# Performance work log

Measured on AMD Instinct MI355X. Metric: run time of the kernel, lower is better.

## Reference

```python
import jax, jax.numpy as jnp
import numpy as np

S, B, D, H, FF = 1024, 8, 512, 8, 2048
HD = D // H
ALPHA, BETA = 0.5, 0.5
EPS = 1e-5


def setup_inputs() -> dict:
    key = jax.random.key(0)
    ks = jax.random.split(key, 12)
    rn = lambda k, sh, sc=0.02: jax.random.normal(k, sh, dtype=jnp.float32) * sc
    ln = jnp.stack([jnp.ones(D), jnp.zeros(D), jnp.ones(D), jnp.zeros(D)]).astype(jnp.float32)
    return {
        "src": rn(ks[0], (S, B, D), 1.0),
        "src_depth": rn(ks[1], (S, B, D), 1.0),
        "pos": rn(ks[2], (S, B, D), 1.0),
        "attn_w_img": rn(ks[3], (4, D, D)),
        "attn_b_img": jnp.zeros((4, D), jnp.float32),
        "attn_w_dpt": rn(ks[4], (4, D, D)),
        "attn_b_dpt": jnp.zeros((4, D), jnp.float32),
        "ffn_w1_img": rn(ks[5], (FF, D)),
        "ffn_b1_img": jnp.zeros((FF,), jnp.float32),
        "ffn_w2_img": rn(ks[6], (D, FF)),
        "ffn_b2_img": jnp.zeros((D,), jnp.float32),
        "ffn_w1_dpt": rn(ks[7], (FF, D)),
        "ffn_b1_dpt": jnp.zeros((FF,), jnp.float32),
        "ffn_w2_dpt": rn(ks[8], (D, FF)),
        "ffn_b2_dpt": jnp.zeros((D,), jnp.float32),
        "ln_img": ln,
        "ln_dpt": ln,
    }


def _layer_norm(x, g, b):
    m = jnp.mean(x, axis=-1, keepdims=True)
    v = jnp.var(x, axis=-1, keepdims=True)  # biased, matches torch LayerNorm
    return (x - m) * jax.lax.rsqrt(v + EPS) * g + b


def _heads(t, W, b):  # [B,S,D] x [D,D] -> [B,H,S,hd]  (torch Linear: y = x W^T + b)
    y = jnp.einsum('bsd,ed->bse', t, W) + b
    return y.reshape(B, S, H, HD).transpose(0, 2, 1, 3)


def _forward(src, src_depth, pos, attn_w_img, attn_b_img, attn_w_dpt, attn_b_dpt,
             ffn_w1_img, ffn_b1_img, ffn_w2_img, ffn_b2_img,
             ffn_w1_dpt, ffn_b1_dpt, ffn_w2_dpt, ffn_b2_dpt, ln_img, ln_dpt):
    # seq-first -> batch-first
    x = src.transpose(1, 0, 2)        # [B,S,D]
    xd = src_depth.transpose(1, 0, 2)
    p = pos.transpose(1, 0, 2)
    qk_in = x + p                     # img stream: q = k = src + pos
    # depth stream: pos_depth is None in layer.forward -> no pos embed
    q = _heads(qk_in, attn_w_img[0], attn_b_img[0])
    k = _heads(qk_in, attn_w_img[1], attn_b_img[1])
    v = _heads(x, attn_w_img[2], attn_b_img[2])
    qd = _heads(xd, attn_w_dpt[0], attn_b_dpt[0])
    kd = _heads(xd, attn_w_dpt[1], attn_b_dpt[1])
    vd = _heads(xd, attn_w_dpt[2], attn_b_dpt[2])
    scale = 1.0 / np.sqrt(HD).astype(np.float32)
    a_img = jax.nn.softmax(jnp.einsum('bhld,bhsd->bhls', q, k) * scale, axis=-1)
    a_dpt = jax.nn.softmax(jnp.einsum('bhld,bhsd->bhls', qd, kd) * scale, axis=-1)
    sh_img = (1.0 - ALPHA) * a_img + ALPHA * a_dpt
    sh_dpt = (1.0 - BETA) * a_dpt + BETA * a_img
    o_img = jnp.einsum('bhls,bhsd->bhld', sh_img, v).transpose(0, 2, 1, 3).reshape(B, S, D)
    o_dpt = jnp.einsum('bhls,bhsd->bhld', sh_dpt, vd).transpose(0, 2, 1, 3).reshape(B, S, D)
    o_img = jnp.einsum('bsd,ed->bse', o_img, attn_w_img[3]) + attn_b_img[3]
    o_dpt = jnp.einsum('bsd,ed->bse', o_dpt, attn_w_dpt[3]) + attn_b_dpt[3]
    # img residual + LN + FFN + LN
    x = _layer_norm(x + o_img, ln_img[0], ln_img[1])
    ff = jnp.einsum('bsf,df->bsd',
                    jax.nn.relu(jnp.einsum('bsd,fd->bsf', x, ffn_w1_img) + ffn_b1_img),
                    ffn_w2_img) + ffn_b2_img
    x = _layer_norm(x + ff, ln_img[2], ln_img[3])
    # depth residual + LN + FFN + LN
    xd = _layer_norm(xd + o_dpt, ln_dpt[0], ln_dpt[1])
    ffd = jnp.einsum('bsf,df->bsd',
                     jax.nn.relu(jnp.einsum('bsd,fd->bsf', xd, ffn_w1_dpt) + ffn_b1_dpt),
                     ffn_w2_dpt) + ffn_b2_dpt
    xd = _layer_norm(xd + ffd, ln_dpt[2], ln_dpt[3])
    return x.transpose(1, 0, 2), xd.transpose(1, 0, 2)  # back to [S,B,D]


def reference(src, src_depth, pos, attn_w_img, attn_b_img, attn_w_dpt, attn_b_dpt,
              ffn_w1_img, ffn_b1_img, ffn_w2_img, ffn_b2_img,
              ffn_w1_dpt, ffn_b1_dpt, ffn_w2_dpt, ffn_b2_dpt, ln_img, ln_dpt):
    return _forward(src, src_depth, pos, attn_w_img, attn_b_img, attn_w_dpt, attn_b_dpt,
                    ffn_w1_img, ffn_b1_img, ffn_w2_img, ffn_b2_img,
                    ffn_w1_dpt, ffn_b1_dpt, ffn_w2_dpt, ffn_b2_dpt, ln_img, ln_dpt)
```

## Files before the change

### kernel.cpp

```cpp
#include <hip/hip_runtime.h>
#include <math.h>

#define S_  1024
#define B_  8
#define D_  512
#define H_  8
#define HD_ 64
#define FF_ 2048
#define M_  8192
#define DD_ (D_ * D_)

typedef __attribute__((ext_vector_type(8))) short short8;
typedef __attribute__((ext_vector_type(4))) float f32x4;

static __device__ __forceinline__ unsigned short f2bf(float x) {
  union { float f; unsigned int u; } v; v.f = x;
  unsigned int r = v.u + 0x7fff + ((v.u >> 16) & 1);
  return (unsigned short)(r >> 16);
}
static __device__ __forceinline__ float bf2f(unsigned short x) {
  union { unsigned int u; float f; } v; v.u = ((unsigned int)x) << 16;
  return v.f;
}
static __device__ __forceinline__ unsigned int pack_bf2(float a, float b) {
  union { float f; unsigned int u; } x, y; x.f = a; y.f = b;
  return ((x.u + 0x8000u) >> 16) | ((y.u + 0x8000u) & 0xffff0000u);
}
static __device__ __forceinline__ void gl_lds16(const unsigned short* g, unsigned short* l) {
  __builtin_amdgcn_global_load_lds((__attribute__((address_space(1))) void*)(g),
                                   (__attribute__((address_space(3))) void*)(l), 16, 0, 0);
}

struct CvtJobs { const float* in[6]; unsigned short* out[6]; };
__global__ __launch_bounds__(256) void wcvt_kernel(CvtJobs j) {
  int job = blockIdx.y;
  int i = (blockIdx.x * 256 + threadIdx.x) * 4;
  float4 v = *(const float4*)(j.in[job] + i);
  unsigned short u[4] = {f2bf(v.x), f2bf(v.y), f2bf(v.z), f2bf(v.w)};
  *(uint2*)(j.out[job] + i) = *(const uint2*)u;
}

__global__ __launch_bounds__(256) void acvt_kernel(const float* __restrict__ src,
    const float* __restrict__ srcd, const float* __restrict__ pos,
    unsigned short* __restrict__ src16, unsigned short* __restrict__ srcd16,
    unsigned short* __restrict__ qkin16) {
  int job = blockIdx.y;
  int i = (blockIdx.x * 256 + threadIdx.x) * 4;
  const float* a = (job == 0) ? src : (job == 1) ? srcd : src;
  float4 v = *(const float4*)(a + i);
  if (job == 2) {
    float4 p = *(const float4*)(pos + i);
    v.x += p.x; v.y += p.y; v.z += p.z; v.w += p.w;
  }
  unsigned short* o = (job == 0) ? src16 : (job == 1) ? srcd16 : qkin16;
  unsigned short u[4] = {f2bf(v.x), f2bf(v.y), f2bf(v.z), f2bf(v.w)};
  *(uint2*)(o + i) = *(const uint2*)u;
}

static __device__ __forceinline__ void mgemm_body(
    const unsigned short* __restrict__ X, const unsigned short* __restrict__ W,
    const float* __restrict__ bias, const float* __restrict__ resf,
    const unsigned short* __restrict__ resb, unsigned short* __restrict__ Yb,
    float* __restrict__ Yf, int N, int K, int relu, int bx, int by,
    unsigned short* As, unsigned short* Bs)
{
  int tid = threadIdx.x;
  int lane = tid & 63, w = tid >> 6;
  int ml = lane & 15, g = lane >> 4;
  int wm = w >> 1, wn = w & 1;
  int m0 = by * 128, n0 = bx * 128;

  int lrow = w * 32 + (lane >> 2);
  int lcol = (lane & 3) * 8;
  const unsigned short* gA = X + (size_t)(m0 + lrow) * K + lcol;
  const unsigned short* gB = W + (size_t)(n0 + lrow) * K + lcol;
  unsigned short* lA = As + w * 1024;
  unsigned short* lB = Bs + w * 1024;

  f32x4 acc[4][4];
  #pragma unroll
  for (int i = 0; i < 4; i++)
    #pragma unroll
    for (int j = 0; j < 4; j++) acc[i][j] = (f32x4){0.f, 0.f, 0.f, 0.f};

  for (int k0 = 0; k0 < K; k0 += 32) {
    __syncthreads();
    gl_lds16(gA + k0, lA);
    gl_lds16(gA + k0 + (size_t)16 * K, lA + 512);
    gl_lds16(gB + k0, lB);
    gl_lds16(gB + k0 + (size_t)16 * K, lB + 512);
    __syncthreads();

    short8 af[4], bfr[4];
    #pragma unroll
    for (int i = 0; i < 4; i++)
      af[i] = *(const short8*)&As[(wm * 64 + i * 16 + ml) * 32 + g * 8];
    #pragma unroll
    for (int j = 0; j < 4; j++)
      bfr[j] = *(const short8*)&Bs[(wn * 64 + j * 16 + ml) * 32 + g * 8];
    #pragma unroll
    for (int i = 0; i < 4; i++)
      #pragma unroll
      for (int j = 0; j < 4; j++)
        acc[i][j] = __builtin_amdgcn_mfma_f32_16x16x32_bf16(af[i], bfr[j], acc[i][j], 0, 0, 0);
  }

  #pragma unroll
  for (int i = 0; i < 4; i++) {
    int grow = m0 + wm * 64 + i * 16 + g * 4;
    #pragma unroll
    for (int j = 0; j < 4; j++) {
      int gcol = n0 + wn * 64 + j * 16 + ml;
      float bv = bias[gcol];
      #pragma unroll
      for (int r = 0; r < 4; r++) {
        size_t idx = (size_t)(grow + r) * N + gcol;
        float v = acc[i][j][r] + bv;
        if (resf) v += resf[idx];
        if (resb) v += bf2f(resb[idx]);
        if (relu) v = fmaxf(v, 0.0f);
        if (Yb) Yb[idx] = f2bf(v);
        if (Yf) Yf[idx] = v;
      }
    }
  }
}

__global__ __launch_bounds__(256) void qkv_kernel(
    const unsigned short* __restrict__ qkin, const unsigned short* __restrict__ src16,
    const unsigned short* __restrict__ srcd16,
    const unsigned short* __restrict__ w_i, const unsigned short* __restrict__ w_d,
    const float* __restrict__ bA_i, const float* __restrict__ bA_d,
    unsigned short* __restrict__ qkimg, unsigned short* __restrict__ vimg,
    unsigned short* __restrict__ dptqkv)
{
  __shared__ unsigned short As[128 * 32];
  __shared__ unsigned short Bs[128 * 32];
  int bx = blockIdx.x, by = blockIdx.y;
  if (bx < 8)
    mgemm_body(qkin, w_i, bA_i, nullptr, nullptr, qkimg, nullptr, 1024, 512, 0, bx, by, As, Bs);
  else if (bx < 12)
    mgemm_body(src16, w_i + 2 * DD_, bA_i + 1024, nullptr, nullptr, vimg, nullptr, 512, 512, 0, bx - 8, by, As, Bs);
  else
    mgemm_body(srcd16, w_d, bA_d, nullptr, nullptr, dptqkv, nullptr, 1536, 512, 0, bx - 12, by, As, Bs);
}

__global__ __launch_bounds__(256) void pgemm_kernel(
    const unsigned short* __restrict__ X0, const unsigned short* __restrict__ X1,
    const unsigned short* __restrict__ W0, const unsigned short* __restrict__ W1,
    const float* __restrict__ b0, const float* __restrict__ b1,
    const float* __restrict__ rf0, const float* __restrict__ rf1,
    const unsigned short* __restrict__ rb0, const unsigned short* __restrict__ rb1,
    unsigned short* __restrict__ Y0, unsigned short* __restrict__ Y1,
    int N, int K, int relu)
{
  __shared__ unsigned short As[128 * 32];
  __shared__ unsigned short Bs[128 * 32];
  int z = blockIdx.z;
  mgemm_body(z ? X1 : X0, z ? W1 : W0, z ? b1 : b0, z ? rf1 : rf0,
             z ? rb1 : rb0, z ? Y1 : Y0, nullptr, N, K, relu,
             blockIdx.x, blockIdx.y, As, Bs);
}

__global__ __launch_bounds__(256) void vtrans_kernel(
    const unsigned short* __restrict__ v0, int ld0, unsigned short* __restrict__ vt0,
    const unsigned short* __restrict__ v1, int ld1, unsigned short* __restrict__ vt1)
{
  __shared__ unsigned short tile[64][72];
  const unsigned short* v = blockIdx.z ? v1 : v0;
  unsigned short* vt = blockIdx.z ? vt1 : vt0;
  int ld = blockIdx.z ? ld1 : ld0;
  int bh = blockIdx.y, b = bh >> 3, h = bh & 7;
  int s0 = blockIdx.x * 64;
  int tid = threadIdx.x;
  #pragma unroll
  for (int t = 0; t < 2; t++) {
    int idx = t * 256 + tid;
    int i = idx >> 3, c8 = (idx & 7) * 8;
    *(uint4*)&tile[i][c8] =
        *(const uint4*)(v + ((size_t)(s0 + i) * B_ + b) * ld + h * HD_ + c8);
  }
  __syncthreads();
  int hd = tid >> 2, j0 = (tid & 3) * 16;
  unsigned short tmp[16];
  #pragma unroll
  for (int j = 0; j < 16; j++) tmp[j] = tile[j0 + j][hd];
  unsigned short* dst = vt + ((size_t)bh * HD_ + hd) * S_ + s0 + j0;
  *(uint4*)(dst) = *(const uint4*)&tmp[0];
  *(uint4*)(dst + 8) = *(const uint4*)&tmp[8];
}

__global__ __launch_bounds__(256) void ln16_kernel(
    const unsigned short* __restrict__ X0, const unsigned short* __restrict__ X1,
    unsigned short* __restrict__ Yb0, unsigned short* __restrict__ Yb1,
    float* __restrict__ Yf0, float* __restrict__ Yf1,
    const float* __restrict__ gb0, const float* __restrict__ gb1)
{
  int row = blockIdx.x, tid = threadIdx.x;
  int strm = row >> 13, r = row & 8191;
  const unsigned short* X = strm ? X1 : X0;
  unsigned short* Yb = strm ? Yb1 : Yb0;
  float* Yf = strm ? Yf1 : Yf0;
  const float* gb = strm ? gb1 : gb0;

  ushort2 xv = *(const ushort2*)(X + (size_t)r * D_ + 2 * tid);
  float v0 = bf2f(xv.x), v1 = bf2f(xv.y);
  float s = v0 + v1, q = v0 * v0 + v1 * v1;
  #pragma unroll
  for (int msk = 1; msk < 64; msk <<= 1) {
    s += __shfl_xor(s, msk);
    q += __shfl_xor(q, msk);
  }
  __shared__ float ss[4], qs[4];
  int wid = tid >> 6;
  if ((tid & 63) == 0) { ss[wid] = s; qs[wid] = q; }
  __syncthreads();
  s = ss[0] + ss[1] + ss[2] + ss[3];
  q = qs[0] + qs[1] + qs[2] + qs[3];
  float mean = s * (1.0f / D_);
  float var  = q * (1.0f / D_) - mean * mean;
  float inv  = rsqrtf(var + 1e-5f);
  float2 gg = *(const float2*)(gb + 2 * tid);
  float2 bb = *(const float2*)(gb + 512 + 2 * tid);
  float o0 = (v0 - mean) * inv * gg.x + bb.x;
  float o1 = (v1 - mean) * inv * gg.y + bb.y;
  if (Yb) {
    unsigned int pk = pack_bf2(o0, o1);
    unsigned short u[2] = {f2bf(o0), f2bf(o1)};
    *(unsigned int*)(Yb + (size_t)r * D_ + 2 * tid) = *(const unsigned int*)u;
    (void)pk;
  }
  if (Yf) {
    float2 o; o.x = o0; o.y = o1;
    *(float2*)(Yf + (size_t)r * D_ + 2 * tid) = o;
  }
}

__global__ __launch_bounds__(256, 2) void attn_kernel(
    const unsigned short* __restrict__ Qi, const unsigned short* __restrict__ Ki, int ldi,
    const unsigned short* __restrict__ Vti,
    const unsigned short* __restrict__ Qd, const unsigned short* __restrict__ Kd, int ldd,
    const unsigned short* __restrict__ Vtd,
    unsigned short* __restrict__ oi, unsigned short* __restrict__ od)
{
  __shared__ __align__(16) unsigned short Kls[2][64 * 64];
  __shared__ __align__(16) unsigned short Vls[2][64 * 64];
  __shared__ __align__(16) unsigned short Pl[4][2][16 * 80];

  int tid = threadIdx.x;
  int bh = blockIdx.y, b = bh >> 3, h = bh & 7;
  int q0 = blockIdx.x * 128;
  int lane = tid & 63, w = tid >> 6;
  int ml = lane & 15, g = lane >> 4;
  int mx = ml & 7;

  short8 qf[2][2][2];
  #pragma unroll
  for (int t = 0; t < 2; t++) {
    size_t tok = (size_t)(q0 + w * 32 + t * 16 + ml) * B_ + b;
    const unsigned short* qa_i = Qi + tok * ldi + h * HD_ + g * 8;
    const unsigned short* qa_d = Qd + tok * ldd + h * HD_ + g * 8;
    qf[t][0][0] = *(const short8*)(qa_i);  qf[t][0][1] = *(const short8*)(qa_i + 32);
    qf[t][1][0] = *(const short8*)(qa_d);  qf[t][1][1] = *(const short8*)(qa_d + 32);
  }

  int srow = lane >> 3;
  int chg = (lane & 7) ^ srow;
  const unsigned short* gbase; size_t s1, s2; unsigned short* lbase;
  if (w == 0)      { gbase = Ki  + ((size_t)srow * B_ + b) * ldi + h * HD_ + chg * 8; s1 = (size_t)B_ * ldi; s2 = s1; lbase = &Kls[0][0]; }
  else if (w == 1) { gbase = Kd  + ((size_t)srow * B_ + b) * ldd + h * HD_ + chg * 8; s1 = (size_t)B_ * ldd; s2 = s1; lbase = &Kls[1][0]; }
  else if (w == 2) { gbase = Vti + (size_t)bh * HD_ * S_ + (size_t)srow * S_ + chg * 8; s1 = S_; s2 = 1; lbase = &Vls[0][0]; }
  else             { gbase = Vtd + (size_t)bh * HD_ * S_ + (size_t)srow * S_ + chg * 8; s1 = S_; s2 = 1; lbase = &Vls[1][0]; }

  f32x4 acc4[2][4][4];
  #pragma unroll
  for (int t = 0; t < 2; t++)
    #pragma unroll
    for (int cb = 0; cb < 4; cb++)
      #pragma unroll
      for (int n = 0; n < 4; n++) acc4[t][cb][n] = (f32x4){0.f, 0.f, 0.f, 0.f};
  float lI[2] = {0.f, 0.f}, lD[2] = {0.f, 0.f};
  const float scale = 0.125f;

  for (int kt = 0; kt < S_ / 64; kt++) {
    int k0 = kt * 64;
    __syncthreads();
    {
      const unsigned short* gp = gbase + (size_t)k0 * s2;
      #pragma unroll
      for (int rr = 0; rr < 8; rr++)
        gl_lds16(gp + (size_t)rr * 8 * s1, lbase + rr * 512);
    }
    __syncthreads();

    #pragma unroll
    for (int t = 0; t < 2; t++) {
      #pragma unroll
      for (int st = 0; st < 2; st++) {
        float* ls = st ? &lD[t] : &lI[t];
        const unsigned short* Kt = &Kls[st][0];
        #pragma unroll
        for (int n = 0; n < 4; n++) {
          int rbase = (n * 16 + ml) * 64;
          short8 kf0 = *(const short8*)&Kt[rbase + ((g ^ mx) * 8)];
          short8 kf1 = *(const short8*)&Kt[rbase + (((g + 4) ^ mx) * 8)];
          f32x4 a = (f32x4){0.f, 0.f, 0.f, 0.f};
          a = __builtin_amdgcn_mfma_f32_16x16x32_bf16(kf0, qf[t][st][0], a, 0, 0, 0);
          a = __builtin_amdgcn_mfma_f32_16x16x32_bf16(kf1, qf[t][st][1], a, 0, 0, 0);
          float p0 = __expf(a[0] * scale), p1 = __expf(a[1] * scale);
          float p2 = __expf(a[2] * scale), p3 = __expf(a[3] * scale);
          *ls += (p0 + p1) + (p2 + p3);
          uint2 pk; pk.x = pack_bf2(p0, p1); pk.y = pack_bf2(p2, p3);
          *(uint2*)&Pl[w][st][ml * 80 + n * 16 + g * 4] = pk;
        }
      }
      #pragma unroll
      for (int c = 0; c < 2; c++) {
        short8 pI = *(const short8*)&Pl[w][0][ml * 80 + g * 8 + c * 32];
        short8 pD = *(const short8*)&Pl[w][1][ml * 80 + g * 8 + c * 32];
        #pragma unroll
        for (int n = 0; n < 4; n++) {
          int rbase = (n * 16 + ml) * 64;
          int sc = (((g + 4 * c) ^ mx)) * 8;
          short8 vI = *(const short8*)&Vls[0][rbase + sc];
          short8 vD = *(const short8*)&Vls[1][rbase + sc];
          acc4[t][0][n] = __builtin_amdgcn_mfma_f32_16x16x32_bf16(pI, vI, acc4[t][0][n], 0, 0, 0);
          acc4[t][1][n] = __builtin_amdgcn_mfma_f32_16x16x32_bf16(pD, vI, acc4[t][1][n], 0, 0, 0);
          acc4[t][2][n] = __builtin_amdgcn_mfma_f32_16x16x32_bf16(pI, vD, acc4[t][2][n], 0, 0, 0);
          acc4[t][3][n] = __builtin_amdgcn_mfma_f32_16x16x32_bf16(pD, vD, acc4[t][3][n], 0, 0, 0);
        }
      }
    }
  }

  #pragma unroll
  for (int t = 0; t < 2; t++) {
    lI[t] += __shfl_xor(lI[t], 16);  lI[t] += __shfl_xor(lI[t], 32);
    lD[t] += __shfl_xor(lD[t], 16);  lD[t] += __shfl_xor(lD[t], 32);
  }
  #pragma unroll
  for (int t = 0; t < 2; t++) {
    float invI = 1.0f / lI[t], invD = 1.0f / lD[t];
    #pragma unroll
    for (int r = 0; r < 4; r++) {
      float iI = __shfl(invI, g * 4 + r, 16);
      float iD = __shfl(invD, g * 4 + r, 16);
      int qrow = q0 + w * 32 + t * 16 + g * 4 + r;
      size_t ob = ((size_t)qrow * B_ + b) * D_ + h * HD_;
      #pragma unroll
      for (int n = 0; n < 4; n++) {
        oi[ob + n * 16 + ml] = f2bf(0.5f * (acc4[t][0][n][r] * iI + acc4[t][1][n][r] * iD));
        od[ob + n * 16 + ml] = f2bf(0.5f * (acc4[t][3][n][r] * iD + acc4[t][2][n][r] * iI));
      }
    }
  }
}

extern "C" void kernel_launch(void* const* d_in, const int* in_sizes, int n_in,
                              void* d_out, int out_size, void* d_ws, size_t ws_size,
                              hipStream_t stream) {
  const float* src  = (const float*)d_in[0];
  const float* srcd = (const float*)d_in[1];
  const float* pos  = (const float*)d_in[2];
  const float* wA_i = (const float*)d_in[3];
  const float* bA_i = (const float*)d_in[4];
  const float* wA_d = (const float*)d_in[5];
  const float* bA_d = (const float*)d_in[6];
  const float* w1_i = (const float*)d_in[7];
  const float* b1_i = (const float*)d_in[8];
  const float* w2_i = (const float*)d_in[9];
  const float* b2_i = (const float*)d_in[10];
  const float* w1_d = (const float*)d_in[11];
  const float* b1_d = (const float*)d_in[12];
  const float* w2_d = (const float*)d_in[13];
  const float* b2_d = (const float*)d_in[14];
  const float* ln_i = (const float*)d_in[15];
  const float* ln_d = (const float*)d_in[16];

  float* out = (float*)d_out;
  unsigned short* u = (unsigned short*)d_ws;
  const size_t T4 = (size_t)M_ * D_;
  const size_t WSZ = (size_t)FF_ * D_;

  unsigned short* src16  = u;
  unsigned short* srcd16 = u + T4;
  unsigned short* qkimg  = u + 2 * T4;
  unsigned short* vimg   = u + 4 * T4;
  unsigned short* dptqkv = u + 5 * T4;
  unsigned short* w_i16  = u + 8 * T4;
  unsigned short* w_d16  = w_i16 + WSZ;
  unsigned short* w1i16  = w_d16 + WSZ;
  unsigned short* w2i16  = w1i16 + WSZ;
  unsigned short* w1d16  = w2i16 + WSZ;
  unsigned short* w2d16  = w1d16 + WSZ;
  unsigned short* t16_i  = w2d16 + WSZ;
  unsigned short* t16_d  = t16_i + T4;
  unsigned short* x16_i  = t16_d + T4;
  unsigned short* x16_d  = x16_i + T4;
  unsigned short* vt_i   = src16;
  unsigned short* vt_d   = srcd16;
  unsigned short* h16_i  = u;
  unsigned short* h16_d  = u + 4 * T4;
  unsigned short* qkin16 = (unsigned short*)out;
  unsigned short* oi16   = (unsigned short*)out;
  unsigned short* od16   = (unsigned short*)out + T4;

  dim3 blk(256);

  CvtJobs cj;
  cj.in[0] = wA_i; cj.out[0] = w_i16;
  cj.in[1] = wA_d; cj.out[1] = w_d16;
  cj.in[2] = w1_i; cj.out[2] = w1i16;
  cj.in[3] = w2_i; cj.out[3] = w2i16;
  cj.in[4] = w1_d; cj.out[4] = w1d16;
  cj.in[5] = w2_d; cj.out[5] = w2d16;
  wcvt_kernel<<<dim3(1024, 6), blk, 0, stream>>>(cj);
  acvt_kernel<<<dim3(4096, 3), blk, 0, stream>>>(src, srcd, pos, src16, srcd16, qkin16);

  qkv_kernel<<<dim3(24, 64), blk, 0, stream>>>(qkin16, src16, srcd16, w_i16, w_d16,
                                               bA_i, bA_d, qkimg, vimg, dptqkv);
  vtrans_kernel<<<dim3(16, 64, 2), blk, 0, stream>>>(vimg, 512, vt_i, dptqkv + 1024, 1536, vt_d);

  attn_kernel<<<dim3(S_ / 128, B_ * H_), blk, 0, stream>>>(
      qkimg, qkimg + 512, 1024, vt_i, dptqkv, dptqkv + 512, 1536, vt_d, oi16, od16);

  pgemm_kernel<<<dim3(4, 64, 2), blk, 0, stream>>>(
      oi16, od16, w_i16 + 3 * DD_, w_d16 + 3 * DD_, bA_i + 1536, bA_d + 1536,
      src, srcd, nullptr, nullptr, t16_i, t16_d, 512, 512, 0);
  ln16_kernel<<<2 * M_, blk, 0, stream>>>(t16_i, t16_d, x16_i, x16_d,
                                          nullptr, nullptr, ln_i, ln_d);
  pgemm_kernel<<<dim3(16, 64, 2), blk, 0, stream>>>(
      x16_i, x16_d, w1i16, w1d16, b1_i, b1_d,
      nullptr, nullptr, nullptr, nullptr, h16_i, h16_d, 2048, 512, 1);
  pgemm_kernel<<<dim3(4, 64, 2), blk, 0, stream>>>(
      h16_i, h16_d, w2i16, w2d16, b2_i, b2_d,
      nullptr, nullptr, x16_i, x16_d, t16_i, t16_d, 512, 2048, 0);
  ln16_kernel<<<2 * M_, blk, 0, stream>>>(t16_i, t16_d, nullptr, nullptr,
                                          out, out + T4, ln_i + 2 * D_, ln_d + 2 * D_);
}
```

Baseline: 470.3 us.

## Double-buffer GEMM LDS tiles with BK=64, XOR swizzle, and retune P-tile padding

The shared GEMM body now loads 64-wide K tiles into two LDS buffers, issuing the next tile's global-to-LDS copy before computing on the current one. This halves the barrier count per K and overlaps memory with MFMA work. An XOR swizzle on the column chunk is meant to avoid LDS bank conflicts. The attention kernel's P scratch row stride drops from 80 to 72. LDS use for the GEMMs grows fourfold (64 KB per block), which may reduce occupancy.

```diff
diff --git a/kernel.cpp b/kernel.cpp
--- a/kernel.cpp
+++ b/kernel.cpp
@@ -70,12 +70,12 @@
   int wm = w >> 1, wn = w & 1;
   int m0 = by * 128, n0 = bx * 128;
 
-  int lrow = w * 32 + (lane >> 2);
-  int lcol = (lane & 3) * 8;
+  int lrow = tid >> 3;
+  int lcol = ((tid & 7) ^ (lrow & 7)) * 8;
   const unsigned short* gA = X + (size_t)(m0 + lrow) * K + lcol;
   const unsigned short* gB = W + (size_t)(n0 + lrow) * K + lcol;
-  unsigned short* lA = As + w * 1024;
-  unsigned short* lB = Bs + w * 1024;
+  unsigned short* lA = As + w * 512;
+  unsigned short* lB = Bs + w * 512;
 
   f32x4 acc[4][4];
   #pragma unroll
@@ -83,26 +83,49 @@
     #pragma unroll
     for (int j = 0; j < 4; j++) acc[i][j] = (f32x4){0.f, 0.f, 0.f, 0.f};
 
-  for (int k0 = 0; k0 < K; k0 += 32) {
+  int NT = K >> 6;
+
+  auto STAGE = [&](int buf, int k0) {
+    const unsigned short* ga = gA + k0;
+    const unsigned short* gb = gB + k0;
+    unsigned short* la = lA + buf * 8192;
+    unsigned short* lb = lB + buf * 8192;
+    #pragma unroll
+    for (int rr = 0; rr < 4; rr++) {
+      gl_lds16(ga + (size_t)rr * 32 * K, la + rr * 2048);
+      gl_lds16(gb + (size_t)rr * 32 * K, lb + rr * 2048);
+    }
+  };
+
+  STAGE(0, 0);
+  __syncthreads();
+
+  for (int kt = 0; kt < NT; kt++) {
+    int cur = kt & 1;
+    if (kt + 1 < NT) STAGE(cur ^ 1, (kt + 1) * 64);
+
+    const unsigned short* lAc = As + cur * 8192;
+    const unsigned short* lBc = Bs + cur * 8192;
+    #pragma unroll
+    for (int ks = 0; ks < 2; ks++) {
+      short8 af[4], bfr[4];
+      #pragma unroll
+      for (int i = 0; i < 4; i++) {
+        int r = wm * 64 + i * 16 + ml;
+        af[i] = *(const short8*)&lAc[r * 64 + (((ks * 4 + g) ^ (r & 7)) * 8)];
+      }
+      #pragma unroll
+      for (int j = 0; j < 4; j++) {
+        int r = wn * 64 + j * 16 + ml;
+        bfr[j] = *(const short8*)&lBc[r * 64 + (((ks * 4 + g) ^ (r & 7)) * 8)];
+      }
+      #pragma unroll
+      for (int i = 0; i < 4; i++)
+        #pragma unroll
+        for (int j = 0; j < 4; j++)
+          acc[i][j] = __builtin_amdgcn_mfma_f32_16x16x32_bf16(af[i], bfr[j], acc[i][j], 0, 0, 0);
+    }
     __syncthreads();
-    gl_lds16(gA + k0, lA);
-    gl_lds16(gA + k0 + (size_t)16 * K, lA + 512);
-    gl_lds16(gB + k0, lB);
-    gl_lds16(gB + k0 + (size_t)16 * K, lB + 512);
-    __syncthreads();
-
-    short8 af[4], bfr[4];
-    #pragma unroll
-    for (int i = 0; i < 4; i++)
-      af[i] = *(const short8*)&As[(wm * 64 + i * 16 + ml) * 32 + g * 8];
-    #pragma unroll
-    for (int j = 0; j < 4; j++)
-      bfr[j] = *(const short8*)&Bs[(wn * 64 + j * 16 + ml) * 32 + g * 8];
-    #pragma unroll
-    for (int i = 0; i < 4; i++)
-      #pragma unroll
-      for (int j = 0; j < 4; j++)
-        acc[i][j] = __builtin_amdgcn_mfma_f32_16x16x32_bf16(af[i], bfr[j], acc[i][j], 0, 0, 0);
   }
 
   #pragma unroll
@@ -134,8 +157,8 @@
     unsigned short* __restrict__ qkimg, unsigned short* __restrict__ vimg,
     unsigned short* __restrict__ dptqkv)
 {
-  __shared__ unsigned short As[128 * 32];
-  __shared__ unsigned short Bs[128 * 32];
+  __shared__ unsigned short As[2 * 128 * 64];
+  __shared__ unsigned short Bs[2 * 128 * 64];
   int bx = blockIdx.x, by = blockIdx.y;
   if (bx < 8)
     mgemm_body(qkin, w_i, bA_i, nullptr, nullptr, qkimg, nullptr, 1024, 512, 0, bx, by, As, Bs);
@@ -154,8 +177,8 @@
     unsigned short* __restrict__ Y0, unsigned short* __restrict__ Y1,
     int N, int K, int relu)
 {
-  __shared__ unsigned short As[128 * 32];
-  __shared__ unsigned short Bs[128 * 32];
+  __shared__ unsigned short As[2 * 128 * 64];
+  __shared__ unsigned short Bs[2 * 128 * 64];
   int z = blockIdx.z;
   mgemm_body(z ? X1 : X0, z ? W1 : W0, z ? b1 : b0, z ? rf1 : rf0,
              z ? rb1 : rb0, z ? Y1 : Y0, nullptr, N, K, relu,
@@ -245,7 +268,7 @@
 {
   __shared__ __align__(16) unsigned short Kls[2][64 * 64];
   __shared__ __align__(16) unsigned short Vls[2][64 * 64];
-  __shared__ __align__(16) unsigned short Pl[4][2][16 * 80];
+  __shared__ __align__(16) unsigned short Pl[4][2][16 * 72];
 
   int tid = threadIdx.x;
   int bh = blockIdx.y, b = bh >> 3, h = bh & 7;
@@ -311,13 +334,13 @@
           float p2 = __expf(a[2] * scale), p3 = __expf(a[3] * scale);
           *ls += (p0 + p1) + (p2 + p3);
           uint2 pk; pk.x = pack_bf2(p0, p1); pk.y = pack_bf2(p2, p3);
-          *(uint2*)&Pl[w][st][ml * 80 + n * 16 + g * 4] = pk;
+          *(uint2*)&Pl[w][st][ml * 72 + n * 16 + g * 4] = pk;
         }
       }
       #pragma unroll
       for (int c = 0; c < 2; c++) {
-        short8 pI = *(const short8*)&Pl[w][0][ml * 80 + g * 8 + c * 32];
-        short8 pD = *(const short8*)&Pl[w][1][ml * 80 + g * 8 + c * 32];
+        short8 pI = *(const short8*)&Pl[w][0][ml * 72 + g * 8 + c * 32];
+        short8 pD = *(const short8*)&Pl[w][1][ml * 72 + g * 8 + c * 32];
         #pragma unroll
         for (int n = 0; n < 4; n++) {
           int rbase = (n * 16 + ml) * 64;
```

After: 452.8 us. 1.04x faster.
